# Kernel optimization log

Measured on AMD Instinct MI355X. Metric: run time of the kernel, lower is better.

The kernel has to match this reference:

```python
import jax, jax.numpy as jnp
import numpy as np

B, T, C = 2, 2048, 1024
H = 16
D = C // H  # head_dim = 64


def setup_inputs() -> dict:
    key = jax.random.key(0)
    k1, k2, k3, k4, k5 = jax.random.split(key, 5)
    s = 1.0 / np.sqrt(C)
    return {
        "x": jax.random.normal(k1, (B, T, C), dtype=jnp.float32),
        "w_qkv": jax.random.normal(k2, (C, 3 * C), dtype=jnp.float32) * s,
        "b_qkv": jax.random.normal(k3, (3 * C,), dtype=jnp.float32) * 0.01,
        "w_out": jax.random.normal(k4, (C, C), dtype=jnp.float32) * s,
        "b_out": jax.random.normal(k5, (C,), dtype=jnp.float32) * 0.01,
    }


def reference(x, w_qkv, b_qkv, w_out, b_out):
    Bx, Tx, Cx = x.shape
    qkv = x @ w_qkv + b_qkv                      # [B,T,3C]
    qkv = qkv.reshape(Bx, Tx, 3, H, D)
    q, k, v = qkv[:, :, 0], qkv[:, :, 1], qkv[:, :, 2]  # [B,T,H,D]
    # [B,H,T,T] scores with scaling
    scores = jnp.einsum("bqhd,bkhd->bhqk", q, k) / np.sqrt(D).astype(np.float32)
    causal = jnp.tril(jnp.ones((Tx, Tx), dtype=bool))
    scores = jnp.where(causal[None, None], scores, -jnp.inf)
    attn = jax.nn.softmax(scores, axis=-1)
    out = jnp.einsum("bhqk,bkhd->bqhd", attn, v).reshape(Bx, Tx, Cx)
    return out @ w_out + b_out
```

## Files before the change

### kernel.cpp

```cpp
#include <hip/hip_runtime.h>
#include <stdint.h>

typedef unsigned short u16;
typedef __attribute__((ext_vector_type(8))) short bfrag;
typedef __attribute__((ext_vector_type(4))) short bfrag4;
typedef __attribute__((ext_vector_type(4))) float f32x4;

#define MFMA_BF16 __builtin_amdgcn_mfma_f32_16x16x32_bf16

static constexpr int Bc = 2;
static constexpr int Tc = 2048;
static constexpr int Cc = 1024;
static constexpr int Hc = 16;
static constexpr int Dc = 64;
static constexpr int N3 = 3 * Cc;

__device__ __forceinline__ u16 f2bf(float f) {
    union { unsigned int i; float f; } v; v.f = f;
    unsigned int u = v.i;
    u += 0x7fffu + ((u >> 16) & 1u);
    return (u16)(u >> 16);
}
__device__ __forceinline__ unsigned int fbits(float f) {
    union { unsigned int i; float f; } v; v.f = f; return v.i;
}
__device__ __forceinline__ unsigned int pack_bf2(float hi, float lo) {
    return __builtin_amdgcn_perm(fbits(hi), fbits(lo), 0x07060302u);
}

#if __has_builtin(__builtin_amdgcn_mfma_f32_16x16x16bf16_1k)
__device__ __forceinline__ f32x4 MFMA16(bfrag4 a, bfrag4 b, f32x4 c) {
    return __builtin_amdgcn_mfma_f32_16x16x16bf16_1k(a, b, c, 0, 0, 0);
}
#elif __has_builtin(__builtin_amdgcn_mfma_f32_16x16x16_bf16)
__device__ __forceinline__ f32x4 MFMA16(bfrag4 a, bfrag4 b, f32x4 c) {
    return __builtin_amdgcn_mfma_f32_16x16x16_bf16(a, b, c, 0, 0, 0);
}
#else
__device__ __forceinline__ f32x4 MFMA16(bfrag4 a, bfrag4 b, f32x4 c) {
    bfrag a8 = {a[0], a[1], a[2], a[3], 0, 0, 0, 0};
    bfrag b8 = {b[0], b[1], b[2], b[3], 0, 0, 0, 0};
    return MFMA_BF16(a8, b8, c, 0, 0, 0);
}
#endif

__device__ __forceinline__ void async_load16(const u16* g, u16* lds) {
    __builtin_amdgcn_global_load_lds(
        (const __attribute__((address_space(1))) unsigned int*)g,
        (__attribute__((address_space(3))) unsigned int*)lds, 16, 0, 0);
}

__global__ __launch_bounds__(256) void prep(
    const float* __restrict__ x, const float* __restrict__ w_qkv,
    const float* __restrict__ w_out, u16* __restrict__ xb,
    u16* __restrict__ WqkvT, u16* __restrict__ WoutT) {
    __shared__ u16 tile[32][33];
    const int blk = blockIdx.x, tid = threadIdx.x;
    if (blk < 4096) {
        const int i = (blk * 256 + tid) * 4;
        const float4 v = *(const float4*)(x + i);
        ushort4 o;
        o.x = f2bf(v.x); o.y = f2bf(v.y); o.z = f2bf(v.z); o.w = f2bf(v.w);
        *(ushort4*)(xb + i) = o;
        return;
    }
    const float* in; u16* out; int rows, cols, c0, r0;
    if (blk < 4096 + 3072) {
        const int t = blk - 4096;
        in = w_qkv; out = WqkvT; rows = 1024; cols = 3072;
        c0 = (t % 96) * 32; r0 = (t / 96) * 32;
    } else {
        const int t = blk - 7168;
        in = w_out; out = WoutT; rows = 1024; cols = 1024;
        c0 = (t & 31) * 32; r0 = (t >> 5) * 32;
    }
    const int row = tid >> 3;
    const int cg  = (tid & 7) * 4;
    const float4 v = *(const float4*)(in + (size_t)(r0 + row) * cols + c0 + cg);
    tile[cg + 0][row] = f2bf(v.x);
    tile[cg + 1][row] = f2bf(v.y);
    tile[cg + 2][row] = f2bf(v.z);
    tile[cg + 3][row] = f2bf(v.w);
    __syncthreads();
    const int tx = tid & 31, ty = tid >> 5;
    for (int i = 0; i < 4; i++)
        out[(size_t)(c0 + ty + 8 * i) * rows + r0 + tx] = tile[ty + 8 * i][tx];
}

__global__ __launch_bounds__(512, 2) void gemm_qkv(
    const u16* __restrict__ A, const u16* __restrict__ BT,
    const float* __restrict__ bias, u16* __restrict__ outQK,
    u16* __restrict__ Vt) {
    constexpr int Kd = 1024, Nn = 3072, Td = 32;
    extern __shared__ __align__(16) u16 smem[];
    u16* As = smem;
    u16* Bs = smem + 4 * (128 * 32);

    const int tid  = threadIdx.x;
    const int wave = tid >> 6, lane = tid & 63;
    const int quad = lane >> 4, l16 = lane & 15;
    const int wm = wave >> 2, wn = wave & 3;
    const int m0 = blockIdx.y * 128, n0 = blockIdx.x * 384;

    f32x4 acc[4][6];
    #pragma unroll
    for (int i = 0; i < 4; i++)
        #pragma unroll
        for (int j = 0; j < 6; j++)
            acc[i][j] = (f32x4){0.f, 0.f, 0.f, 0.f};

    const int rloc = 2 * (lane >> 3) + ((lane >> 2) & 1);
    const int cg   = ((lane & 3) ^ ((lane >> 3) & 3)) * 8;
    const int rk   = (l16 >> 1) & 3;
    const int rodd = (l16 & 1) * 32;

    const u16* Ag = A  + (size_t)(m0 + wave * 16 + rloc) * Kd + cg;
    const u16* Bg = BT + (size_t)(n0 + wave * 48 + rloc) * Kd + cg;
    u16* ldsA = As + (wave * 16) * 32;
    u16* ldsB = Bs + (wave * 48) * 32;

    int offA[4], offB[6];
    #pragma unroll
    for (int mt = 0; mt < 4; mt++) {
        const int r = wm * 64 + mt * 16 + l16;
        offA[mt] = (r >> 1) * 64 + rodd + (quad ^ rk) * 8;
    }
    #pragma unroll
    for (int nt = 0; nt < 6; nt++) {
        const int r = wn * 96 + nt * 16 + l16;
        offB[nt] = (r >> 1) * 64 + rodd + (quad ^ rk) * 8;
    }

    #define GLD_A(h, bsel)                                                     \
        async_load16(Ag + ((h) << 5), ldsA + (bsel) * (128 * 32));
    #define GLD_B(h, bsel, j)                                                  \
        async_load16(Bg + (size_t)((j) * 16) * Kd + ((h) << 5),                \
                     ldsB + (bsel) * (384 * 32) + (j) * (16 * 32));

    #pragma unroll
    for (int h = 0; h < 3; h++) {
        GLD_A(h, h);
        GLD_B(h, h, 0); GLD_B(h, h, 1); GLD_B(h, h, 2);
    }
    asm volatile("s_waitcnt vmcnt(8)" ::: "memory");
    __builtin_amdgcn_s_barrier();
    asm volatile("" ::: "memory");

    for (int h = 0; h < Td; h++) {
        const int bsel = h & 3;
        const u16* Ab = As + bsel * (128 * 32);
        const u16* Bb = Bs + bsel * (384 * 32);
        const int psel = (h + 3) & 3;

        bfrag af[4], bf0[3];
        #pragma unroll
        for (int mt = 0; mt < 4; mt++) af[mt] = *(const bfrag*)(Ab + offA[mt]);
        #pragma unroll
        for (int nt = 0; nt < 3; nt++) bf0[nt] = *(const bfrag*)(Bb + offB[nt]);
        if (h + 3 < Td) { GLD_A(h + 3, psel); GLD_B(h + 3, psel, 0); }
        __builtin_amdgcn_s_barrier();
        asm volatile("s_waitcnt lgkmcnt(0)" ::: "memory");
        __builtin_amdgcn_sched_barrier(0);
        __builtin_amdgcn_s_setprio(1);
        #pragma unroll
        for (int mt = 0; mt < 4; mt++)
            #pragma unroll
            for (int nt = 0; nt < 3; nt++)
                acc[mt][nt] = MFMA_BF16(af[mt], bf0[nt], acc[mt][nt], 0, 0, 0);
        __builtin_amdgcn_s_setprio(0);
        __builtin_amdgcn_s_barrier();
        asm volatile("" ::: "memory");

        bfrag bf1[3];
        #pragma unroll
        for (int nt = 0; nt < 3; nt++)
            bf1[nt] = *(const bfrag*)(Bb + offB[nt + 3]);
        if (h + 3 < Td) { GLD_B(h + 3, psel, 1); GLD_B(h + 3, psel, 2); }
        if (h <= Td - 4)      asm volatile("s_waitcnt vmcnt(8)" ::: "memory");
        else if (h == Td - 3) asm volatile("s_waitcnt vmcnt(4)" ::: "memory");
        else if (h == Td - 2) asm volatile("s_waitcnt vmcnt(0)" ::: "memory");
        __builtin_amdgcn_s_barrier();
        asm volatile("s_waitcnt lgkmcnt(0)" ::: "memory");
        __builtin_amdgcn_sched_barrier(0);
        __builtin_amdgcn_s_setprio(1);
        #pragma unroll
        for (int mt = 0; mt < 4; mt++)
            #pragma unroll
            for (int nt = 0; nt < 3; nt++)
                acc[mt][nt + 3] = MFMA_BF16(af[mt], bf1[nt], acc[mt][nt + 3], 0, 0, 0);
        __builtin_amdgcn_s_setprio(0);
        __builtin_amdgcn_s_barrier();
        asm volatile("" ::: "memory");
    }
    #undef GLD_A
    #undef GLD_B

    #pragma unroll
    for (int nt = 0; nt < 6; nt++) {
        const int gn = n0 + wn * 96 + nt * 16 + l16;
        const float bv = bias[gn];
        if (gn < 2 * Cc) {
            const float scl = (gn < Cc) ? 0.125f : 1.0f;
            #pragma unroll
            for (int mt = 0; mt < 4; mt++) {
                #pragma unroll
                for (int r = 0; r < 4; r++) {
                    const int gm = m0 + wm * 64 + mt * 16 + quad * 4 + r;
                    outQK[(size_t)gm * Nn + gn] = f2bf((acc[mt][nt][r] + bv) * scl);
                }
            }
        } else {
            const int gnv = gn - 2 * Cc;
            const int h = gnv >> 6, d = gnv & 63;
            #pragma unroll
            for (int mt = 0; mt < 4; mt++) {
                const int gmb = m0 + wm * 64 + mt * 16 + quad * 4;
                const int b = gmb >> 11, trow = gmb & (Tc - 1);
                ushort4 o;
                o.x = f2bf(acc[mt][nt][0] + bv);
                o.y = f2bf(acc[mt][nt][1] + bv);
                o.z = f2bf(acc[mt][nt][2] + bv);
                o.w = f2bf(acc[mt][nt][3] + bv);
                *(ushort4*)(Vt + ((size_t)((b * Hc + h) * Dc + d)) * Tc + trow) = o;
            }
        }
    }
}

__global__ __launch_bounds__(512, 2) void gemm_out(
    const u16* __restrict__ A, const u16* __restrict__ BT,
    const float* __restrict__ bias, float* __restrict__ out,
    int M, int Nn, int K) {
    extern __shared__ __align__(16) u16 smem[];
    u16* As = smem;
    u16* Bs = smem + 3 * (128 * 32);

    const int tid  = threadIdx.x;
    const int wave = tid >> 6, lane = tid & 63;
    const int quad = lane >> 4, l16 = lane & 15;
    const int wm = wave >> 2, wn = wave & 3;
    const int m0 = blockIdx.y * 128, n0 = blockIdx.x * 128;

    f32x4 acc[4][2];
    #pragma unroll
    for (int i = 0; i < 4; i++)
        #pragma unroll
        for (int j = 0; j < 2; j++)
            acc[i][j] = (f32x4){0.f, 0.f, 0.f, 0.f};

    const int rA = lane >> 2;
    const int cA = ((lane & 3) ^ (rA & 3)) * 8;

    const u16* Ag = A  + (size_t)(m0 + wave * 16 + rA) * K + cA;
    const u16* Bg = BT + (size_t)(n0 + wave * 16 + rA) * K + cA;
    u16* ldsA = As + (wave * 16) * 32;
    u16* ldsB = Bs + (wave * 16) * 32;

    const int swz8 = (quad ^ (l16 & 3)) * 8;
    int offA[4], offB[2];
    #pragma unroll
    for (int mt = 0; mt < 4; mt++)
        offA[mt] = (wm * 64 + mt * 16 + l16) * 32 + swz8;
    #pragma unroll
    for (int nt = 0; nt < 2; nt++)
        offB[nt] = (wn * 32 + nt * 16 + l16) * 32 + swz8;

    #define STAGE_O(t, bsel)                                                   \
        {                                                                      \
            const int k0_ = (t) << 5;                                          \
            async_load16(Ag + k0_, ldsA + (bsel) * (128 * 32));                \
            async_load16(Bg + k0_, ldsB + (bsel) * (128 * 32));                \
        }

    STAGE_O(0, 0);
    STAGE_O(1, 1);

    const int T = K >> 5;
    for (int t = 0; t < T; t++) {
        if (t + 1 < T) asm volatile("s_waitcnt vmcnt(2)" ::: "memory");
        else           asm volatile("s_waitcnt vmcnt(0)" ::: "memory");
        __builtin_amdgcn_s_barrier();
        asm volatile("" ::: "memory");
        if (t + 2 < T) { STAGE_O(t + 2, (t + 2) % 3); }

        const u16* Ab = As + (t % 3) * (128 * 32);
        const u16* Bb = Bs + (t % 3) * (128 * 32);
        bfrag af[4], bf[2];
        #pragma unroll
        for (int mt = 0; mt < 4; mt++) af[mt] = *(const bfrag*)(Ab + offA[mt]);
        #pragma unroll
        for (int nt = 0; nt < 2; nt++) bf[nt] = *(const bfrag*)(Bb + offB[nt]);

        __builtin_amdgcn_s_setprio(1);
        #pragma unroll
        for (int mt = 0; mt < 4; mt++)
            #pragma unroll
            for (int nt = 0; nt < 2; nt++)
                acc[mt][nt] = MFMA_BF16(af[mt], bf[nt], acc[mt][nt], 0, 0, 0);
        __builtin_amdgcn_s_setprio(0);
    }
    #undef STAGE_O

    #pragma unroll
    for (int nt = 0; nt < 2; nt++) {
        const int gn = n0 + wn * 32 + nt * 16 + l16;
        const float bv = bias[gn];
        #pragma unroll
        for (int mt = 0; mt < 4; mt++) {
            #pragma unroll
            for (int r = 0; r < 4; r++) {
                const int gm = m0 + wm * 64 + mt * 16 + quad * 4 + r;
                out[(size_t)gm * Nn + gn] = acc[mt][nt][r] + bv;
            }
        }
    }
}

__global__ __launch_bounds__(256, 3) void attn_kernel(
    const u16* __restrict__ QKVp, const u16* __restrict__ Vt,
    u16* __restrict__ Ob) {
    __shared__ __align__(16) u16 KsF[2][64 * 64];
    __shared__ __align__(16) u16 VsF[2][64 * 64];

    const int tid  = threadIdx.x;
    const int wave = tid >> 6, lane = tid & 63;
    const int quad = lane >> 4, l16 = lane & 15;

    const int bh = blockIdx.x & 31;
    const int g5 = blockIdx.x >> 5;
    const int jq = (g5 < 8) ? 31 - g5
                 : (g5 < 16) ? g5 + 8
                 : (g5 < 24) ? 31 - g5
                 : g5 - 24;
    const int b = bh >> 4, h = bh & 15;
    const u16* Qp = QKVp + (size_t)b * Tc * N3 + h * Dc;
    const u16* Kp = Qp + Cc;
    const u16* Vp = Vt + (size_t)bh * Dc * Tc;

    const int row8 = lane >> 3;
    const int swz  = ((lane & 7) ^ row8) * 8;
    const int pk0 = ((quad)     ^ (l16 & 7)) * 8;
    const int pk1 = ((quad + 4) ^ (l16 & 7)) * 8;
    const int vc = ((2 * wave + (quad >> 1)) ^ (l16 & 7)) * 8 + (quad & 1) * 4;

    bfrag qf0[4], qf1[4];
    #pragma unroll
    for (int qg = 0; qg < 4; qg++) {
        const u16* qp = Qp + (size_t)(jq * 64 + qg * 16 + l16) * N3 + quad * 8;
        qf0[qg] = *(const bfrag*)qp;
        qf1[qg] = *(const bfrag*)(qp + 32);
    }

    float l4[4] = {0.f, 0.f, 0.f, 0.f};
    f32x4 oacc[4][4];
    #pragma unroll
    for (int qg = 0; qg < 4; qg++)
        #pragma unroll
        for (int ng = 0; ng < 4; ng++)
            oacc[qg][ng] = (f32x4){0.f, 0.f, 0.f, 0.f};

    #define STAGEKV(t, bsel)                                                    \
        {                                                                       \
            const int k0_ = (t) * 64;                                           \
            _Pragma("unroll")                                                   \
            for (int j = 0; j < 2; j++) {                                       \
                const int rr = wave * 16 + j * 8;                               \
                const int gr = rr + row8;                                       \
                async_load16(Kp + (size_t)(k0_ + gr) * N3 + swz,                \
                             &KsF[bsel][rr * 64]);                              \
                async_load16(Vp + (size_t)gr * Tc + k0_ + swz,                  \
                             &VsF[bsel][rr * 64]);                              \
            }                                                                   \
        }

    STAGEKV(0, 0);
    for (int t = 0; t <= jq; t++) {
        __syncthreads();
        if (t < jq) STAGEKV(t + 1, (t + 1) & 1);
        const u16* Kb = KsF[t & 1];
        const u16* Vb = VsF[t & 1];

        const u16* kb = Kb + (wave * 16 + l16) * 64;
        bfrag kf0 = *(const bfrag*)(kb + pk0);
        bfrag kf1 = *(const bfrag*)(kb + pk1);

        f32x4 s[4];
        __builtin_amdgcn_s_setprio(1);
        #pragma unroll
        for (int qg = 0; qg < 4; qg++) {
            f32x4 z = (f32x4){0.f, 0.f, 0.f, 0.f};
            z = MFMA_BF16(kf0, qf0[qg], z, 0, 0, 0);
            z = MFMA_BF16(kf1, qf1[qg], z, 0, 0, 0);
            s[qg] = z;
        }
        __builtin_amdgcn_s_setprio(0);

        #pragma unroll
        for (int qg = 0; qg < 4; qg++)
            #pragma unroll
            for (int r = 0; r < 4; r++)
                s[qg][r] = __expf(s[qg][r]);
        if (t == jq) {
            #pragma unroll
            for (int qg = 0; qg < 4; qg++)
                #pragma unroll
                for (int r = 0; r < 4; r++)
                    if (wave * 16 + quad * 4 + r > qg * 16 + l16) s[qg][r] = 0.f;
        }
        #pragma unroll
        for (int qg = 0; qg < 4; qg++)
            l4[qg] += s[qg][0] + s[qg][1] + s[qg][2] + s[qg][3];

        bfrag4 vf[4];
        #pragma unroll
        for (int ng = 0; ng < 4; ng++)
            vf[ng] = *(const bfrag4*)(Vb + (ng * 16 + l16) * 64 + vc);

        __builtin_amdgcn_s_setprio(1);
        #pragma unroll
        for (int qg = 0; qg < 4; qg++) {
            union { unsigned int u[2]; bfrag4 v; } pf;
            pf.u[0] = pack_bf2(s[qg][1], s[qg][0]);
            pf.u[1] = pack_bf2(s[qg][3], s[qg][2]);
            #pragma unroll
            for (int ng = 0; ng < 4; ng++)
                oacc[qg][ng] = MFMA16(vf[ng], pf.v, oacc[qg][ng]);
        }
        __builtin_amdgcn_s_setprio(0);
    }
    #undef STAGEKV

    __syncthreads();

    float* lred = (float*)VsF;
    #pragma unroll
    for (int qg = 0; qg < 4; qg++)
        lred[(wave * 4 + qg) * 64 + lane] = l4[qg];
    __syncthreads();
    float inv[4];
    #pragma unroll
    for (int qg = 0; qg < 4; qg++) {
        float ls = lred[(0 * 4 + qg) * 64 + lane] + lred[(1 * 4 + qg) * 64 + lane]
                 + lred[(2 * 4 + qg) * 64 + lane] + lred[(3 * 4 + qg) * 64 + lane];
        ls += __shfl_xor(ls, 16);
        ls += __shfl_xor(ls, 32);
        inv[qg] = 1.f / ls;
    }

    f32x4* ored = (f32x4*)KsF;
    #pragma unroll
    for (int qg = 0; qg < 4; qg++) {
        __syncthreads();
        #pragma unroll
        for (int ng = 0; ng < 4; ng++)
            ored[(wave * 4 + ng) * 64 + lane] = oacc[qg][ng];
        __syncthreads();
        f32x4 a0 = ored[(0 * 4 + wave) * 64 + lane];
        f32x4 a1 = ored[(1 * 4 + wave) * 64 + lane];
        f32x4 a2 = ored[(2 * 4 + wave) * 64 + lane];
        f32x4 a3 = ored[(3 * 4 + wave) * 64 + lane];
        const int q = jq * 64 + qg * 16 + l16;
        u16* orow = Ob + (size_t)(b * Tc + q) * Cc + h * Dc + wave * 16 + quad * 4;
        ushort4 o;
        o.x = f2bf((a0[0] + a1[0] + a2[0] + a3[0]) * inv[qg]);
        o.y = f2bf((a0[1] + a1[1] + a2[1] + a3[1]) * inv[qg]);
        o.z = f2bf((a0[2] + a1[2] + a2[2] + a3[2]) * inv[qg]);
        o.w = f2bf((a0[3] + a1[3] + a2[3] + a3[3]) * inv[qg]);
        *(ushort4*)orow = o;
    }
}

extern "C" void kernel_launch(void* const* d_in, const int* in_sizes, int n_in,
                              void* d_out, int out_size, void* d_ws, size_t ws_size,
                              hipStream_t stream) {
    const float* x     = (const float*)d_in[0];
    const float* w_qkv = (const float*)d_in[1];
    const float* b_qkv = (const float*)d_in[2];
    const float* w_out = (const float*)d_in[3];
    const float* b_out = (const float*)d_in[4];
    float* out = (float*)d_out;
    u16* ws  = (u16*)d_ws;

    u16* xb    = ws;
    u16* WqkvT = xb    + (size_t)4096 * 1024;
    u16* WoutT = WqkvT + (size_t)3072 * 1024;
    u16* QKVp  = WoutT + (size_t)1024 * 1024;
    u16* Vt    = QKVp  + (size_t)4096 * 3072;
    u16* Ao    = xb;

    static bool smem_set = false;
    if (!smem_set) {
        hipFuncSetAttribute(reinterpret_cast<const void*>(gemm_qkv),
                            hipFuncAttributeMaxDynamicSharedMemorySize,
                            128 * 1024);
        hipFuncSetAttribute(reinterpret_cast<const void*>(gemm_out),
                            hipFuncAttributeMaxDynamicSharedMemorySize,
                            48 * 1024);
        smem_set = true;
    }

    prep<<<8192, 256, 0, stream>>>(x, w_qkv, w_out, xb, WqkvT, WoutT);
    gemm_qkv<<<dim3(3072 / 384, 4096 / 128), 512, 128 * 1024, stream>>>(
        xb, WqkvT, b_qkv, QKVp, Vt);
    attn_kernel<<<1024, 256, 0, stream>>>(QKVp, Vt, Ao);
    gemm_out<<<dim3(1024 / 128, 4096 / 128), 512, 48 * 1024, stream>>>(
        Ao, WoutT, b_out, out, 4096, 1024, 1024);
}
```

Measured before the change: 168.5 us.

## Retile QKV GEMM to 128x192 tiles with K=64 steps and 3-stage pipeline

Rewrites the QKV projection GEMM to use 128x192 output tiles, so twice as many blocks run (512 vs 256). Each k-step now covers 64 instead of 32, with a new XOR swizzle for the LDS layout. The 4-buffer, split-half pipeline becomes a 3-buffer pipeline with a single barrier-and-compute phase per step. The goals are better occupancy across CUs and fewer barriers per unit of K. In exchange, each block reuses its A tile across fewer columns, and launch bounds now drop to one block per CU.

```diff
diff --git a/kernel.cpp b/kernel.cpp
--- a/kernel.cpp
+++ b/kernel.cpp
@@ -87,78 +87,79 @@
         out[(size_t)(c0 + ty + 8 * i) * rows + r0 + tx] = tile[ty + 8 * i][tx];
 }
 
-__global__ __launch_bounds__(512, 2) void gemm_qkv(
+__global__ __launch_bounds__(512, 1) void gemm_qkv(
     const u16* __restrict__ A, const u16* __restrict__ BT,
     const float* __restrict__ bias, u16* __restrict__ outQK,
     u16* __restrict__ Vt) {
-    constexpr int Kd = 1024, Nn = 3072, Td = 32;
+    constexpr int Kd = 1024, Nn = 3072, Td = 16;
     extern __shared__ __align__(16) u16 smem[];
     u16* As = smem;
-    u16* Bs = smem + 4 * (128 * 32);
+    u16* Bs = smem + 3 * (128 * 64);
 
     const int tid  = threadIdx.x;
     const int wave = tid >> 6, lane = tid & 63;
     const int quad = lane >> 4, l16 = lane & 15;
     const int wm = wave >> 2, wn = wave & 3;
-    const int m0 = blockIdx.y * 128, n0 = blockIdx.x * 384;
-
-    f32x4 acc[4][6];
+    const int m0 = blockIdx.y * 128, n0 = blockIdx.x * 192;
+
+    f32x4 acc[4][3];
     #pragma unroll
     for (int i = 0; i < 4; i++)
         #pragma unroll
-        for (int j = 0; j < 6; j++)
+        for (int j = 0; j < 3; j++)
             acc[i][j] = (f32x4){0.f, 0.f, 0.f, 0.f};
 
-    const int rloc = 2 * (lane >> 3) + ((lane >> 2) & 1);
-    const int cg   = ((lane & 3) ^ ((lane >> 3) & 3)) * 8;
-    const int rk   = (l16 >> 1) & 3;
-    const int rodd = (l16 & 1) * 32;
-
-    const u16* Ag = A  + (size_t)(m0 + wave * 16 + rloc) * Kd + cg;
-    const u16* Bg = BT + (size_t)(n0 + wave * 48 + rloc) * Kd + cg;
-    u16* ldsA = As + (wave * 16) * 32;
-    u16* ldsB = Bs + (wave * 48) * 32;
-
-    int offA[4], offB[6];
-    #pragma unroll
-    for (int mt = 0; mt < 4; mt++) {
-        const int r = wm * 64 + mt * 16 + l16;
-        offA[mt] = (r >> 1) * 64 + rodd + (quad ^ rk) * 8;
-    }
-    #pragma unroll
-    for (int nt = 0; nt < 6; nt++) {
-        const int r = wn * 96 + nt * 16 + l16;
-        offB[nt] = (r >> 1) * 64 + rodd + (quad ^ rk) * 8;
-    }
-
-    #define GLD_A(h, bsel)                                                     \
-        async_load16(Ag + ((h) << 5), ldsA + (bsel) * (128 * 32));
+    const int r8   = lane >> 3;
+    const int cswz = ((lane & 7) ^ r8) * 8;
+
+    const u16* Ag = A  + (size_t)(m0 + wave * 16 + r8) * Kd + cswz;
+    const u16* Bg = BT + (size_t)(n0 + wave * 24 + r8) * Kd + cswz;
+    u16* ldsA = As + (wave * 16) * 64;
+    u16* ldsB = Bs + (wave * 24) * 64;
+
+    const int pk0 = ((quad)     ^ (l16 & 7)) * 8;
+    const int pk1 = ((quad + 4) ^ (l16 & 7)) * 8;
+    int offA[4], offB[3];
+    #pragma unroll
+    for (int mt = 0; mt < 4; mt++)
+        offA[mt] = (wm * 64 + mt * 16 + l16) * 64;
+    #pragma unroll
+    for (int nt = 0; nt < 3; nt++)
+        offB[nt] = (wn * 48 + nt * 16 + l16) * 64;
+
+    #define GLD_A(h, bsel, j)                                                  \
+        async_load16(Ag + (size_t)((j) * 8) * Kd + ((h) << 6),                 \
+                     ldsA + (bsel) * (128 * 64) + (j) * (8 * 64));
     #define GLD_B(h, bsel, j)                                                  \
-        async_load16(Bg + (size_t)((j) * 16) * Kd + ((h) << 5),                \
-                     ldsB + (bsel) * (384 * 32) + (j) * (16 * 32));
-
-    #pragma unroll
-    for (int h = 0; h < 3; h++) {
-        GLD_A(h, h);
-        GLD_B(h, h, 0); GLD_B(h, h, 1); GLD_B(h, h, 2);
-    }
-    asm volatile("s_waitcnt vmcnt(8)" ::: "memory");
-    __builtin_amdgcn_s_barrier();
-    asm volatile("" ::: "memory");
+        async_load16(Bg + (size_t)((j) * 8) * Kd + ((h) << 6),                 \
+                     ldsB + (bsel) * (192 * 64) + (j) * (8 * 64));
+    #define STAGE_H(h, bsel)                                                   \
+        { GLD_A(h, bsel, 0); GLD_A(h, bsel, 1);                                \
+          GLD_B(h, bsel, 0); GLD_B(h, bsel, 1); GLD_B(h, bsel, 2); }
+
+    STAGE_H(0, 0);
+    STAGE_H(1, 1);
 
     for (int h = 0; h < Td; h++) {
-        const int bsel = h & 3;
-        const u16* Ab = As + bsel * (128 * 32);
-        const u16* Bb = Bs + bsel * (384 * 32);
-        const int psel = (h + 3) & 3;
-
-        bfrag af[4], bf0[3];
-        #pragma unroll
-        for (int mt = 0; mt < 4; mt++) af[mt] = *(const bfrag*)(Ab + offA[mt]);
-        #pragma unroll
-        for (int nt = 0; nt < 3; nt++) bf0[nt] = *(const bfrag*)(Bb + offB[nt]);
-        if (h + 3 < Td) { GLD_A(h + 3, psel); GLD_B(h + 3, psel, 0); }
+        if (h <= Td - 2) asm volatile("s_waitcnt vmcnt(5)" ::: "memory");
+        else             asm volatile("s_waitcnt vmcnt(0)" ::: "memory");
         __builtin_amdgcn_s_barrier();
+        asm volatile("" ::: "memory");
+        if (h + 2 < Td) { STAGE_H(h + 2, (h + 2) % 3); }
+
+        const u16* Ab = As + (h % 3) * (128 * 64);
+        const u16* Bb = Bs + (h % 3) * (192 * 64);
+        bfrag af0[4], af1[4], bf0[3], bf1[3];
+        #pragma unroll
+        for (int mt = 0; mt < 4; mt++) {
+            af0[mt] = *(const bfrag*)(Ab + offA[mt] + pk0);
+            af1[mt] = *(const bfrag*)(Ab + offA[mt] + pk1);
+        }
+        #pragma unroll
+        for (int nt = 0; nt < 3; nt++) {
+            bf0[nt] = *(const bfrag*)(Bb + offB[nt] + pk0);
+            bf1[nt] = *(const bfrag*)(Bb + offB[nt] + pk1);
+        }
         asm volatile("s_waitcnt lgkmcnt(0)" ::: "memory");
         __builtin_amdgcn_sched_barrier(0);
         __builtin_amdgcn_s_setprio(1);
@@ -166,38 +167,23 @@
         for (int mt = 0; mt < 4; mt++)
             #pragma unroll
             for (int nt = 0; nt < 3; nt++)
-                acc[mt][nt] = MFMA_BF16(af[mt], bf0[nt], acc[mt][nt], 0, 0, 0);
+                acc[mt][nt] = MFMA_BF16(af0[mt], bf0[nt], acc[mt][nt], 0, 0, 0);
+        #pragma unroll
+        for (int mt = 0; mt < 4; mt++)
+            #pragma unroll
+            for (int nt = 0; nt < 3; nt++)
+                acc[mt][nt] = MFMA_BF16(af1[mt], bf1[nt], acc[mt][nt], 0, 0, 0);
         __builtin_amdgcn_s_setprio(0);
         __builtin_amdgcn_s_barrier();
         asm volatile("" ::: "memory");
-
-        bfrag bf1[3];
-        #pragma unroll
-        for (int nt = 0; nt < 3; nt++)
-            bf1[nt] = *(const bfrag*)(Bb + offB[nt + 3]);
-        if (h + 3 < Td) { GLD_B(h + 3, psel, 1); GLD_B(h + 3, psel, 2); }
-        if (h <= Td - 4)      asm volatile("s_waitcnt vmcnt(8)" ::: "memory");
-        else if (h == Td - 3) asm volatile("s_waitcnt vmcnt(4)" ::: "memory");
-        else if (h == Td - 2) asm volatile("s_waitcnt vmcnt(0)" ::: "memory");
-        __builtin_amdgcn_s_barrier();
-        asm volatile("s_waitcnt lgkmcnt(0)" ::: "memory");
-        __builtin_amdgcn_sched_barrier(0);
-        __builtin_amdgcn_s_setprio(1);
-        #pragma unroll
-        for (int mt = 0; mt < 4; mt++)
-            #pragma unroll
-            for (int nt = 0; nt < 3; nt++)
-                acc[mt][nt + 3] = MFMA_BF16(af[mt], bf1[nt], acc[mt][nt + 3], 0, 0, 0);
-        __builtin_amdgcn_s_setprio(0);
-        __builtin_amdgcn_s_barrier();
-        asm volatile("" ::: "memory");
     }
     #undef GLD_A
     #undef GLD_B
-
-    #pragma unroll
-    for (int nt = 0; nt < 6; nt++) {
-        const int gn = n0 + wn * 96 + nt * 16 + l16;
+    #undef STAGE_H
+
+    #pragma unroll
+    for (int nt = 0; nt < 3; nt++) {
+        const int gn = n0 + wn * 48 + nt * 16 + l16;
         const float bv = bias[gn];
         if (gn < 2 * Cc) {
             const float scl = (gn < Cc) ? 0.125f : 1.0f;
@@ -492,7 +478,7 @@
     if (!smem_set) {
         hipFuncSetAttribute(reinterpret_cast<const void*>(gemm_qkv),
                             hipFuncAttributeMaxDynamicSharedMemorySize,
-                            128 * 1024);
+                            120 * 1024);
         hipFuncSetAttribute(reinterpret_cast<const void*>(gemm_out),
                             hipFuncAttributeMaxDynamicSharedMemorySize,
                             48 * 1024);
@@ -500,7 +486,7 @@
     }
 
     prep<<<8192, 256, 0, stream>>>(x, w_qkv, w_out, xb, WqkvT, WoutT);
-    gemm_qkv<<<dim3(3072 / 384, 4096 / 128), 512, 128 * 1024, stream>>>(
+    gemm_qkv<<<dim3(3072 / 192, 4096 / 128), 512, 120 * 1024, stream>>>(
         xb, WqkvT, b_qkv, QKVp, Vt);
     attn_kernel<<<1024, 256, 0, stream>>>(QKVp, Vt, Ao);
     gemm_out<<<dim3(1024 / 128, 4096 / 128), 512, 48 * 1024, stream>>>(
```

New measurement: 171.4 us. No clear change (+1.7%).
